# Optimization experiments

Measured on AMD Instinct MI355X. Metric: run time of the kernel, lower is better.

## Reference

```python
import jax, jax.numpy as jnp
import numpy as np

N = 8192
IN_F = 512
OUT_F = 64
ALPHA = 0.2        # LeakyReLU slope
L_ITERS = 3        # RobustSum iterations
EPS = 0.01
GAMMA = 4.0
T = 1.0
NEG_BIG = -9e15


def setup_inputs() -> dict:
    key = jax.random.key(0)
    k1, k2, k3, k4 = jax.random.split(key, 4)
    x = jax.random.normal(k1, (N, IN_F), dtype=jnp.float32)
    adj = jax.random.randint(k2, (N, N), 0, 2, dtype=jnp.int32)
    # xavier-uniform-like init scales
    limW = 1.414 * np.sqrt(6.0 / (IN_F + OUT_F))
    W = jax.random.uniform(k3, (IN_F, OUT_F), dtype=jnp.float32, minval=-limW, maxval=limW)
    lima = 1.414 * np.sqrt(6.0 / (2 * OUT_F + 1))
    a = jax.random.uniform(k4, (2 * OUT_F, 1), dtype=jnp.float32, minval=-lima, maxval=lima)
    return {"adj": adj, "input": x, "W": W, "a": a}


def _robust_sum_mcp(A, V):
    # M = A @ V, then IRLS-style reweighted aggregation (norm='MCP')
    M = A @ V
    for _ in range(L_ITERS):
        Md = jax.lax.stop_gradient(M)
        Vd = jax.lax.stop_gradient(V)
        # pairwise Euclidean distance [N, N] (fused form of torch.cdist)
        d2 = (jnp.sum(Md * Md, axis=1, keepdims=True)
              + jnp.sum(Vd * Vd, axis=1)[None, :]
              - 2.0 * (Md @ Vd.T))
        dist = jnp.sqrt(jnp.maximum(d2, 0.0))
        w = 1.0 / (dist + EPS) - 1.0 / GAMMA
        w = jnp.maximum(w, EPS)          # w[w < eps] = eps
        ww = w * A
        denom = jnp.maximum(jnp.sum(jnp.abs(ww), axis=-1, keepdims=True), 1e-12)
        ww_norm = ww / denom             # F.normalize(p=1, dim=-1)
        M = (1.0 - T) * M + T * (ww_norm @ V)
    return M


def reference(adj, input, W, a):
    adj_f = adj.astype(jnp.float32)
    h = input @ W                                     # [N, OUT_F]
    a1 = a[:OUT_F, 0]                                 # [OUT_F]
    a2 = a[OUT_F:, 0]                                 # [OUT_F]
    # fused equivalent of cat([h_i, h_j]) @ a : e_ij = lrelu(h_i.a1 + h_j.a2)
    e = jax.nn.leaky_relu((h @ a1)[:, None] + (h @ a2)[None, :], ALPHA)  # [N, N]
    scores = adj_f * e + (1.0 - adj_f) * NEG_BIG
    attention = jax.nn.softmax(scores, axis=1)
    # dropout omitted (eval mode / dropout=0.0)
    h_prime = _robust_sum_mcp(attention, h)
    return jax.nn.elu(h_prime)                        # concat=True
```

## Files before the change

### kernel.cpp

```cpp
#include <hip/hip_runtime.h>
#include <hip/hip_bf16.h>

typedef __attribute__((ext_vector_type(8))) short s8v;
typedef __attribute__((ext_vector_type(4))) short s4v;
typedef __attribute__((ext_vector_type(4))) float f4v;

static __device__ __forceinline__ short f2bf(float f){
  unsigned int u = __float_as_uint(f);
  u = (u + 0x7FFFu + ((u >> 16) & 1u)) >> 16;
  return (short)u;
}

static __device__ __forceinline__ s4v pack4(float a, float b, float c, float d){
  union { s4v v; __hip_bfloat162 h[2]; } u;
  u.h[0] = __float22bfloat162_rn(make_float2(a, b));
  u.h[1] = __float22bfloat162_rn(make_float2(c, d));
  return u.v;
}

static __device__ __forceinline__ f4v mfma16(s4v a, s4v b, f4v c){
  return __builtin_amdgcn_mfma_f32_16x16x16bf16_1k(a, b, c, 0, 0, 0);
}

__global__ __launch_bounds__(256) void k_h(const float* __restrict__ x,
                                           const float* __restrict__ W,
                                           float* __restrict__ h){
  int wid = threadIdx.x >> 6, lane = threadIdx.x & 63;
  int r0 = (blockIdx.x * 4 + wid) * 8;
  const float* xr = x + (size_t)r0 * 512;
  float acc[8] = {0.f,0.f,0.f,0.f,0.f,0.f,0.f,0.f};
  #pragma unroll 4
  for (int k = 0; k < 512; ++k){
    float wv = W[k*64 + lane];
    #pragma unroll
    for (int r = 0; r < 8; ++r)
      acc[r] = fmaf(xr[(size_t)r*512 + k], wv, acc[r]);
  }
  #pragma unroll
  for (int r = 0; r < 8; ++r)
    h[(size_t)(r0 + r)*64 + lane] = acc[r];
}

__global__ __launch_bounds__(256) void k_prep(const float* __restrict__ h,
                                              const float* __restrict__ a,
                                              short* __restrict__ VbfSw,
                                              short* __restrict__ VTsw,
                                              float* __restrict__ F,
                                              float2* __restrict__ EG,
                                              float* __restrict__ V2arr,
                                              float* __restrict__ Pv2,
                                              float* __restrict__ Pg,
                                              float* __restrict__ Vpart){
  __shared__ float t[64][65];
  const int tid = threadIdx.x;
  const int lane = tid & 63, w = tid >> 6;
  const int lo = lane & 15, hi = lane >> 4;
  const int i0 = blockIdx.x * 64;
  #pragma unroll
  for (int it = 0; it < 16; ++it){
    int r = w * 16 + it;
    t[r][lane] = h[(size_t)(i0 + r) * 64 + lane];
  }
  __syncthreads();
  #pragma unroll
  for (int ks = 0; ks < 2; ++ks){
    s8v o;
    #pragma unroll
    for (int e = 0; e < 8; ++e)
      o[e] = f2bf(t[w*16 + lo][ks*32 + hi*8 + e]);
    *(s8v*)(VbfSw + ((size_t)(i0/16 + w)*2 + ks)*512 + lane*8) = o;
  }
  const int p = w >> 1;
  #pragma unroll
  for (int oo = 0; oo < 2; ++oo){
    const int ot = (w & 1) * 2 + oo;
    s8v o;
    #pragma unroll
    for (int e = 0; e < 8; ++e){
      int parity = e >> 2, q = e & 3;
      o[e] = f2bf(t[(p*2 + parity)*16 + hi*4 + q][ot*16 + lo]);
    }
    *(s8v*)(VTsw + ((size_t)(i0/32 + p)*4 + ot)*512 + lane*8) = o;
  }
  if (tid < 64){
    const int r = tid;
    float f = 0.f, g = 0.f, v2 = 0.f;
    #pragma unroll 8
    for (int o = 0; o < 64; ++o){
      float hv = t[r][o];
      f  = fmaf(hv, a[o],      f);
      g  = fmaf(hv, a[64 + o], g);
      v2 = fmaf(hv, hv,        v2);
    }
    const int row = i0 + r;
    F[row] = f;
    V2arr[row] = v2;
    EG[row] = make_float2(__expf(g), __expf(0.2f * g));
    float vmin = v2, gmx = g;
    #pragma unroll
    for (int off = 32; off; off >>= 1){
      vmin = fminf(vmin, __shfl_xor(vmin, off));
      gmx  = fmaxf(gmx,  __shfl_xor(gmx,  off));
    }
    if (r == 0){ Pv2[blockIdx.x] = vmin; Pg[blockIdx.x] = gmx; }
    float cs = 0.f;
    #pragma unroll 8
    for (int rr = 0; rr < 64; ++rr) cs += t[rr][tid];
    Vpart[(size_t)blockIdx.x * 64 + tid] = cs;
  }
}

__global__ __launch_bounds__(512, 4) void k_fused(
    const int* __restrict__ adj,
    const float2* __restrict__ EG, const float* __restrict__ V2arr,
    const float* __restrict__ F,
    const float* __restrict__ Pv2, const float* __restrict__ Pg,
    const float* __restrict__ Vpart,
    const short* __restrict__ VbfSw, const short* __restrict__ VTsw,
    float* __restrict__ out)
{
  __shared__ float numT[8][64][16];
  __shared__ float denL[8][16];
  __shared__ float Mlds[16][68];
  __shared__ float M1L[16][68];
  __shared__ __align__(16) short Mb16[16][64];
  __shared__ float CiL[16], rm2L[16], uaiL[16];
  __shared__ float VmeanL[64];
  __shared__ float gmaxS, v2minS;
  __shared__ int actL, chgL, emptyL;

  const int tid  = threadIdx.x;
  const int w    = tid >> 6;
  const int lane = tid & 63;
  const int lo = lane & 15, hi = lane >> 4;
  const int r0 = blockIdx.x << 4;
  const int i  = r0 + lo;

  if (tid < 64){
    float v = fminf(Pv2[tid], Pv2[tid + 64]);
    float g = fmaxf(Pg[tid],  Pg[tid + 64]);
    #pragma unroll
    for (int off = 32; off; off >>= 1){
      v = fminf(v, __shfl_xor(v, off));
      g = fmaxf(g, __shfl_xor(g, off));
    }
    if (tid == 0){ v2minS = v; gmaxS = g; actL = 0; emptyL = 0; }
  }
  __syncthreads();

  const float fi   = F[i];
  const float gmax = gmaxS;
  const float z    = fi + gmax;
  const float B    = fmaxf(z, 0.2f * z);
  const float e1s  = __expf(fi - B);
  const float e2s  = __expf(0.2f * fi - B);

  const int* arow = adj + (size_t)i * 8192 + hi*4;

  const f4v zero4 = {0.f,0.f,0.f,0.f};
  f4v pacc[4] = {zero4, zero4, zero4, zero4};
  float pden = 0.f;

  for (int c = w; c < 128; c += 8){
    const int* ap = arow + (c << 6);
    s4v wwpk[4];
    #pragma unroll
    for (int nt = 0; nt < 4; ++nt){
      const int jb = (c << 6) + nt*16 + hi*4;
      const int4 av4 = *(const int4*)(ap + nt*16);
      const int ab[4] = {av4.x, av4.y, av4.z, av4.w};
      const f4v u0 = *(const f4v*)(EG + jb);
      const f4v u1 = *(const f4v*)(EG + jb + 2);
      const float ega[4] = {u0[0], u0[2], u1[0], u1[2]};
      const float egb[4] = {u0[1], u0[3], u1[1], u1[3]};
      float wwv[4];
      #pragma unroll
      for (int q = 0; q < 4; ++q){
        float u = fmaxf(e1s * ega[q], e2s * egb[q]);
        u = ab[q] ? u : 0.f;
        pden += u;
        wwv[q] = u;
      }
      wwpk[nt] = pack4(wwv[0], wwv[1], wwv[2], wwv[3]);
    }
    const short* vt = VTsw + (size_t)c*4096 + lane*8;
    #pragma unroll
    for (int p = 0; p < 2; ++p){
      #pragma unroll
      for (int ot = 0; ot < 4; ++ot){
        s8v v8 = *(const s8v*)(vt + (p*4 + ot)*512);
        s4v aLo = {v8[0], v8[1], v8[2], v8[3]};
        s4v aHi = {v8[4], v8[5], v8[6], v8[7]};
        pacc[ot] = mfma16(aLo, wwpk[2*p],   pacc[ot]);
        pacc[ot] = mfma16(aHi, wwpk[2*p+1], pacc[ot]);
      }
    }
  }

  pden += __shfl_xor(pden, 16);
  pden += __shfl_xor(pden, 32);
  if (lane < 16) denL[w][lane] = pden;
  #pragma unroll
  for (int ot = 0; ot < 4; ++ot)
    #pragma unroll
    for (int q = 0; q < 4; ++q)
      numT[w][ot*16 + hi*4 + q][lo] = pacc[ot][q];
  __syncthreads();

  {
    const int ii = tid & 15;
    const int o  = tid >> 4;
    float den = 0.f;
    #pragma unroll
    for (int w2 = 0; w2 < 8; ++w2) den += denL[w2][ii];
    if (o == 0){
      uaiL[ii] = (den <= 0.f) ? (1.0f / 8192.0f) : 0.f;
      if (den <= 0.f) emptyL = 1;
    }
    den = fmaxf(den, 1e-30f);
    const float rden = 1.0f / den;
    #pragma unroll
    for (int rep = 0; rep < 2; ++rep){
      const int oo = o + rep*32;
      float num = 0.f;
      #pragma unroll
      for (int w2 = 0; w2 < 8; ++w2) num += numT[w2][oo][ii];
      Mlds[ii][oo] = num * rden;
    }
    if (tid < 16){
      float fb = F[r0 + tid];
      float zb = fb + gmax;
      float Bb = fmaxf(zb, 0.2f * zb);
      CiL[tid] = Bb + __logf(den);
    }
  }
  __syncthreads();

  if (emptyL){
    if (tid < 64){
      float s = 0.f;
      for (int b = 0; b < 128; ++b) s += Vpart[(size_t)b*64 + tid];
      VmeanL[tid] = s * (1.0f / 8192.0f);
    }
    __syncthreads();
    {
      const int r = tid >> 5, c2 = (tid & 31) << 1;
      if (uaiL[r] > 0.f){ Mlds[r][c2] = VmeanL[c2]; Mlds[r][c2+1] = VmeanL[c2+1]; }
    }
    __syncthreads();
  }

  if (tid < 16){
    float s2 = 0.f;
    #pragma unroll 8
    for (int o = 0; o < 64; ++o) s2 = fmaf(Mlds[tid][o], Mlds[tid][o], s2);
    rm2L[tid] = s2;
    if (sqrtf(s2) > sqrtf(v2minS) - 3.85f) actL = 1;
  }
  __syncthreads();

  if (actL){
    {
      const int r = tid >> 5, c2 = (tid & 31) << 1;
      float a0 = Mlds[r][c2], a1 = Mlds[r][c2+1];
      M1L[r][c2] = a0;  M1L[r][c2+1] = a1;
      Mb16[r][c2] = f2bf(a0); Mb16[r][c2+1] = f2bf(a1);
    }
    const float e1c = __expf(fi - CiL[lo]);
    const float e2c = __expf(0.2f * fi - CiL[lo]);
    const float uai = uaiL[lo];
    __syncthreads();

    for (int pass = 0; pass < 3; ++pass){
      if (tid == 0) chgL = 0;
      __syncthreads();
      const float rm2 = rm2L[lo];
      s8v bM[2];
      #pragma unroll
      for (int ks = 0; ks < 2; ++ks)
        bM[ks] = *(const s8v*)&Mb16[lo][ks*32 + hi*8];

      f4v cacc[4] = {zero4, zero4, zero4, zero4};
      float cden = 0.f;

      for (int c = w; c < 128; c += 8){
        f4v acc[4] = {zero4, zero4, zero4, zero4};
        const short* vb = VbfSw + (size_t)c*4096 + lane*8;
        #pragma unroll
        for (int nt = 0; nt < 4; ++nt){
          #pragma unroll
          for (int ks = 0; ks < 2; ++ks){
            s8v av = *(const s8v*)(vb + (nt*2 + ks)*512);
            acc[nt] = __builtin_amdgcn_mfma_f32_16x16x32_bf16(av, bM[ks], acc[nt], 0, 0, 0);
          }
        }
        f4v d2s[4];
        float dmin = 1e30f;
        #pragma unroll
        for (int nt = 0; nt < 4; ++nt){
          const int jb = (c << 6) + nt*16 + hi*4;
          const f4v v2q = *(const f4v*)(V2arr + jb);
          #pragma unroll
          for (int q = 0; q < 4; ++q){
            float d2 = fmaf(-2.0f, acc[nt][q], rm2 + v2q[q]);
            d2s[nt][q] = d2;
            dmin = fminf(dmin, d2);
          }
        }
        if (__any(dmin < 16.0f)){
          const int* ap = arow + (c << 6);
          s4v wwpk[4];
          #pragma unroll
          for (int nt = 0; nt < 4; ++nt){
            const int jb = (c << 6) + nt*16 + hi*4;
            const int4 av4 = *(const int4*)(ap + nt*16);
            const int ab[4] = {av4.x, av4.y, av4.z, av4.w};
            const f4v u0 = *(const f4v*)(EG + jb);
            const f4v u1 = *(const f4v*)(EG + jb + 2);
            const float ega[4] = {u0[0], u0[2], u1[0], u1[2]};
            const float egb[4] = {u0[1], u0[3], u1[1], u1[3]};
            float wwv[4];
            #pragma unroll
            for (int q = 0; q < 4; ++q){
              float A = fmaxf(e1c * ega[q], e2c * egb[q]);
              A = ab[q] ? A : uai;
              float dist  = sqrtf(fmaxf(d2s[nt][q], 0.f));
              float delta = fmaxf(__builtin_amdgcn_rcpf(dist + 0.01f) - 0.26f, 0.f);
              float ww = delta * A;
              cden += ww;
              wwv[q] = ww;
            }
            wwpk[nt] = pack4(wwv[0], wwv[1], wwv[2], wwv[3]);
          }
          const short* vt = VTsw + (size_t)c*4096 + lane*8;
          #pragma unroll
          for (int p = 0; p < 2; ++p){
            #pragma unroll
            for (int ot = 0; ot < 4; ++ot){
              s8v v8 = *(const s8v*)(vt + (p*4 + ot)*512);
              s4v aLo = {v8[0], v8[1], v8[2], v8[3]};
              s4v aHi = {v8[4], v8[5], v8[6], v8[7]};
              cacc[ot] = mfma16(aLo, wwpk[2*p],   cacc[ot]);
              cacc[ot] = mfma16(aHi, wwpk[2*p+1], cacc[ot]);
            }
          }
        }
      }

      if (__any(cden > 0.f)) chgL = 1;
      __syncthreads();
      if (chgL){
        float cd = cden;
        cd += __shfl_xor(cd, 16);
        cd += __shfl_xor(cd, 32);
        if (lane < 16) denL[w][lane] = cd;
        #pragma unroll
        for (int ot = 0; ot < 4; ++ot)
          #pragma unroll
          for (int q = 0; q < 4; ++q)
            numT[w][ot*16 + hi*4 + q][lo] = cacc[ot][q];
        __syncthreads();
        {
          const int ii = tid & 15;
          const int o  = tid >> 4;
          float den = 0.f;
          #pragma unroll
          for (int w2 = 0; w2 < 8; ++w2) den += denL[w2][ii];
          const float rden = 1.0f / (0.01f + den);
          #pragma unroll
          for (int rep = 0; rep < 2; ++rep){
            const int oo = o + rep*32;
            float num = 0.f;
            #pragma unroll
            for (int w2 = 0; w2 < 8; ++w2) num += numT[w2][oo][ii];
            Mlds[ii][oo] = fmaf(0.01f, M1L[ii][oo], num) * rden;
          }
        }
        __syncthreads();
        {
          const int r = tid >> 5, c2 = (tid & 31) << 1;
          Mb16[r][c2]   = f2bf(Mlds[r][c2]);
          Mb16[r][c2+1] = f2bf(Mlds[r][c2+1]);
        }
        if (tid < 16){
          float s2 = 0.f;
          #pragma unroll 8
          for (int o = 0; o < 64; ++o) s2 = fmaf(Mlds[tid][o], Mlds[tid][o], s2);
          rm2L[tid] = s2;
        }
        __syncthreads();
      }
    }
  }
  __syncthreads();

  #pragma unroll
  for (int rr = 0; rr < 2; ++rr){
    const int ir = w*2 + rr;
    const float v = Mlds[ir][lane];
    out[(size_t)(r0 + ir) * 64 + lane] = (v > 0.f) ? v : (__expf(v) - 1.0f);
  }
}

extern "C" void kernel_launch(void* const* d_in, const int* in_sizes, int n_in,
                              void* d_out, int out_size, void* d_ws, size_t ws_size,
                              hipStream_t stream){
  (void)in_sizes; (void)n_in; (void)out_size; (void)ws_size;
  const int*   adj = (const int*)d_in[0];
  const float* x   = (const float*)d_in[1];
  const float* W   = (const float*)d_in[2];
  const float* a   = (const float*)d_in[3];
  float* out = (float*)d_out;
  char* ws = (char*)d_ws;

  float* h     = (float*)(ws);
  short* VbfSw = (short*)(ws + (2u << 20));
  short* VTsw  = (short*)(ws + (3u << 20));
  float* F     = (float*)(ws + (4u << 20));
  float* V2arr = (float*)(ws + (4u << 20) + (32u << 10));
  float2* EG   = (float2*)(ws + (4u << 20) + (64u << 10));
  float* Vpart = (float*)(ws + (4u << 20) + (128u << 10));
  float* Pv2   = (float*)(ws + (4u << 20) + (160u << 10));
  float* Pg    = (float*)(ws + (4u << 20) + (161u << 10));

  k_h    <<<256, 256, 0, stream>>>(x, W, h);
  k_prep <<<128, 256, 0, stream>>>(h, a, VbfSw, VTsw, F, EG, V2arr, Pv2, Pg, Vpart);
  k_fused<<<512, 512, 0, stream>>>(adj, EG, V2arr, F, Pv2, Pg, Vpart, VbfSw, VTsw, out);
}
```

Baseline: 138.4 us.

## Process 32 rows per block, bit-pack adjacency, reduce partials via LDS atomics

Each block now handles 32 rows with 1024 threads, and every wave computes two 16-row tiles. This lets each loaded V/VT fragment and EG value feed twice as many MFMAs. In the first pass the adjacency rows are packed into 64-bit masks in workspace, so the three IRLS passes read bits instead of re-reading int32 adjacency. Cross-wave reductions use LDS atomicAdd instead of per-wave staging arrays, the pruning threshold changes from 16 to 14.75, and the pass loop exits early when nothing changes. The costs are higher register pressure, atomic contention, a grid of only 256 blocks, and a changed threshold that may affect accuracy.

```diff
diff --git a/kernel.cpp b/kernel.cpp
--- a/kernel.cpp
+++ b/kernel.cpp
@@ -110,21 +110,22 @@
   }
 }
 
-__global__ __launch_bounds__(512, 4) void k_fused(
+__global__ __launch_bounds__(1024, 4) void k_fused(
     const int* __restrict__ adj,
     const float2* __restrict__ EG, const float* __restrict__ V2arr,
     const float* __restrict__ F,
     const float* __restrict__ Pv2, const float* __restrict__ Pg,
     const float* __restrict__ Vpart,
     const short* __restrict__ VbfSw, const short* __restrict__ VTsw,
+    unsigned long long* __restrict__ adjbits,
     float* __restrict__ out)
 {
-  __shared__ float numT[8][64][16];
-  __shared__ float denL[8][16];
-  __shared__ float Mlds[16][68];
-  __shared__ float M1L[16][68];
-  __shared__ __align__(16) short Mb16[16][64];
-  __shared__ float CiL[16], rm2L[16], uaiL[16];
+  __shared__ float Macc[32][65];
+  __shared__ float denA[32];
+  __shared__ float Mlds[32][68];
+  __shared__ float M1L[32][68];
+  __shared__ __align__(16) short Mb16[32][64];
+  __shared__ float CiL[32], rm2L[32], uaiL[32];
   __shared__ float VmeanL[64];
   __shared__ float gmaxS, v2minS;
   __shared__ int actL, chgL, emptyL;
@@ -133,9 +134,15 @@
   const int w    = tid >> 6;
   const int lane = tid & 63;
   const int lo = lane & 15, hi = lane >> 4;
-  const int r0 = blockIdx.x << 4;
-  const int i  = r0 + lo;
-
+  const int r0 = blockIdx.x << 5;
+  const int i0 = r0 + lo;
+  const int i1 = r0 + 16 + lo;
+
+  {
+    float* mz = &Macc[0][0];
+    for (int k2 = tid; k2 < 32*65; k2 += 1024) mz[k2] = 0.f;
+    if (tid < 32) denA[tid] = 0.f;
+  }
   if (tid < 64){
     float v = fminf(Pv2[tid], Pv2[tid + 64]);
     float g = fmaxf(Pg[tid],  Pg[tid + 64]);
@@ -148,41 +155,62 @@
   }
   __syncthreads();
 
-  const float fi   = F[i];
+  const float fi0 = F[i0], fi1 = F[i1];
   const float gmax = gmaxS;
-  const float z    = fi + gmax;
-  const float B    = fmaxf(z, 0.2f * z);
-  const float e1s  = __expf(fi - B);
-  const float e2s  = __expf(0.2f * fi - B);
-
-  const int* arow = adj + (size_t)i * 8192 + hi*4;
+  const float z0 = fi0 + gmax, z1 = fi1 + gmax;
+  const float B0 = fmaxf(z0, 0.2f * z0);
+  const float B1 = fmaxf(z1, 0.2f * z1);
+  const float e1s0 = __expf(fi0 - B0), e2s0 = __expf(0.2f * fi0 - B0);
+  const float e1s1 = __expf(fi1 - B1), e2s1 = __expf(0.2f * fi1 - B1);
+
+  const int* arow0 = adj + (size_t)i0 * 8192 + hi*4;
+  const int* arow1 = adj + (size_t)i1 * 8192 + hi*4;
 
   const f4v zero4 = {0.f,0.f,0.f,0.f};
-  f4v pacc[4] = {zero4, zero4, zero4, zero4};
-  float pden = 0.f;
-
-  for (int c = w; c < 128; c += 8){
-    const int* ap = arow + (c << 6);
-    s4v wwpk[4];
+  f4v pacc0[4] = {zero4, zero4, zero4, zero4};
+  f4v pacc1[4] = {zero4, zero4, zero4, zero4};
+  float pden0 = 0.f, pden1 = 0.f;
+
+  for (int c = w; c < 128; c += 16){
+    const int* ap0 = arow0 + (c << 6);
+    const int* ap1 = arow1 + (c << 6);
+    s4v wp0[4], wp1[4];
+    unsigned long long mrow0 = 0ull, mrow1 = 0ull;
     #pragma unroll
     for (int nt = 0; nt < 4; ++nt){
       const int jb = (c << 6) + nt*16 + hi*4;
-      const int4 av4 = *(const int4*)(ap + nt*16);
-      const int ab[4] = {av4.x, av4.y, av4.z, av4.w};
+      const int4 a0 = *(const int4*)(ap0 + nt*16);
+      const int4 a1 = *(const int4*)(ap1 + nt*16);
       const f4v u0 = *(const f4v*)(EG + jb);
       const f4v u1 = *(const f4v*)(EG + jb + 2);
       const float ega[4] = {u0[0], u0[2], u1[0], u1[2]};
       const float egb[4] = {u0[1], u0[3], u1[1], u1[3]};
-      float wwv[4];
+      const int ab0[4] = {a0.x, a0.y, a0.z, a0.w};
+      const int ab1[4] = {a1.x, a1.y, a1.z, a1.w};
+      float w0v[4], w1v[4];
       #pragma unroll
       for (int q = 0; q < 4; ++q){
-        float u = fmaxf(e1s * ega[q], e2s * egb[q]);
-        u = ab[q] ? u : 0.f;
-        pden += u;
-        wwv[q] = u;
-      }
-      wwpk[nt] = pack4(wwv[0], wwv[1], wwv[2], wwv[3]);
-    }
+        float u = fmaxf(e1s0 * ega[q], e2s0 * egb[q]);
+        u = ab0[q] ? u : 0.f;
+        pden0 += u; w0v[q] = u;
+        float v = fmaxf(e1s1 * ega[q], e2s1 * egb[q]);
+        v = ab1[q] ? v : 0.f;
+        pden1 += v; w1v[q] = v;
+      }
+      const unsigned nib0 = (unsigned)ab0[0] | ((unsigned)ab0[1] << 1)
+                          | ((unsigned)ab0[2] << 2) | ((unsigned)ab0[3] << 3);
+      const unsigned nib1 = (unsigned)ab1[0] | ((unsigned)ab1[1] << 1)
+                          | ((unsigned)ab1[2] << 2) | ((unsigned)ab1[3] << 3);
+      mrow0 |= (unsigned long long)nib0 << (nt*16 + hi*4);
+      mrow1 |= (unsigned long long)nib1 << (nt*16 + hi*4);
+      wp0[nt] = pack4(w0v[0], w0v[1], w0v[2], w0v[3]);
+      wp1[nt] = pack4(w1v[0], w1v[1], w1v[2], w1v[3]);
+    }
+    mrow0 |= __shfl_xor(mrow0, 16); mrow0 |= __shfl_xor(mrow0, 32);
+    mrow1 |= __shfl_xor(mrow1, 16); mrow1 |= __shfl_xor(mrow1, 32);
+    if (hi == 0) adjbits[(size_t)c * 8192 + i0] = mrow0;
+    if (hi == 1) adjbits[(size_t)c * 8192 + i1] = mrow1;
+
     const short* vt = VTsw + (size_t)c*4096 + lane*8;
     #pragma unroll
     for (int p = 0; p < 2; ++p){
@@ -191,47 +219,41 @@
         s8v v8 = *(const s8v*)(vt + (p*4 + ot)*512);
         s4v aLo = {v8[0], v8[1], v8[2], v8[3]};
         s4v aHi = {v8[4], v8[5], v8[6], v8[7]};
-        pacc[ot] = mfma16(aLo, wwpk[2*p],   pacc[ot]);
-        pacc[ot] = mfma16(aHi, wwpk[2*p+1], pacc[ot]);
-      }
-    }
-  }
-
-  pden += __shfl_xor(pden, 16);
-  pden += __shfl_xor(pden, 32);
-  if (lane < 16) denL[w][lane] = pden;
+        pacc0[ot] = mfma16(aLo, wp0[2*p],   pacc0[ot]);
+        pacc0[ot] = mfma16(aHi, wp0[2*p+1], pacc0[ot]);
+        pacc1[ot] = mfma16(aLo, wp1[2*p],   pacc1[ot]);
+        pacc1[ot] = mfma16(aHi, wp1[2*p+1], pacc1[ot]);
+      }
+    }
+  }
+
+  pden0 += __shfl_xor(pden0, 16); pden0 += __shfl_xor(pden0, 32);
+  pden1 += __shfl_xor(pden1, 16); pden1 += __shfl_xor(pden1, 32);
+  if (hi == 0) atomicAdd(&denA[lo],      pden0);
+  if (hi == 1) atomicAdd(&denA[16 + lo], pden1);
   #pragma unroll
   for (int ot = 0; ot < 4; ++ot)
     #pragma unroll
-    for (int q = 0; q < 4; ++q)
-      numT[w][ot*16 + hi*4 + q][lo] = pacc[ot][q];
+    for (int q = 0; q < 4; ++q){
+      atomicAdd(&Macc[lo]     [ot*16 + hi*4 + q], pacc0[ot][q]);
+      atomicAdd(&Macc[16 + lo][ot*16 + hi*4 + q], pacc1[ot][q]);
+    }
   __syncthreads();
 
   {
-    const int ii = tid & 15;
-    const int o  = tid >> 4;
-    float den = 0.f;
-    #pragma unroll
-    for (int w2 = 0; w2 < 8; ++w2) den += denL[w2][ii];
-    if (o == 0){
-      uaiL[ii] = (den <= 0.f) ? (1.0f / 8192.0f) : 0.f;
-      if (den <= 0.f) emptyL = 1;
-    }
-    den = fmaxf(den, 1e-30f);
+    const int r = tid >> 5, cc = (tid & 31) << 1;
+    const float den = fmaxf(denA[r], 1e-30f);
     const float rden = 1.0f / den;
-    #pragma unroll
-    for (int rep = 0; rep < 2; ++rep){
-      const int oo = o + rep*32;
-      float num = 0.f;
-      #pragma unroll
-      for (int w2 = 0; w2 < 8; ++w2) num += numT[w2][oo][ii];
-      Mlds[ii][oo] = num * rden;
-    }
-    if (tid < 16){
-      float fb = F[r0 + tid];
-      float zb = fb + gmax;
-      float Bb = fmaxf(zb, 0.2f * zb);
-      CiL[tid] = Bb + __logf(den);
+    Mlds[r][cc]   = Macc[r][cc]   * rden;
+    Mlds[r][cc+1] = Macc[r][cc+1] * rden;
+    if (tid < 32){
+      const float dn = denA[tid];
+      uaiL[tid] = (dn <= 0.f) ? (1.0f / 8192.0f) : 0.f;
+      if (dn <= 0.f) emptyL = 1;
+      const float fb = F[r0 + tid];
+      const float zb = fb + gmax;
+      const float Bb = fmaxf(zb, 0.2f * zb);
+      CiL[tid] = Bb + __logf(fmaxf(dn, 1e-30f));
     }
   }
   __syncthreads();
@@ -244,13 +266,13 @@
     }
     __syncthreads();
     {
-      const int r = tid >> 5, c2 = (tid & 31) << 1;
-      if (uaiL[r] > 0.f){ Mlds[r][c2] = VmeanL[c2]; Mlds[r][c2+1] = VmeanL[c2+1]; }
+      const int r = tid >> 5, cc = (tid & 31) << 1;
+      if (uaiL[r] > 0.f){ Mlds[r][cc] = VmeanL[cc]; Mlds[r][cc+1] = VmeanL[cc+1]; }
     }
     __syncthreads();
   }
 
-  if (tid < 16){
+  if (tid < 32){
     float s2 = 0.f;
     #pragma unroll 8
     for (int o = 0; o < 64; ++o) s2 = fmaf(Mlds[tid][o], Mlds[tid][o], s2);
@@ -261,76 +283,105 @@
 
   if (actL){
     {
-      const int r = tid >> 5, c2 = (tid & 31) << 1;
-      float a0 = Mlds[r][c2], a1 = Mlds[r][c2+1];
-      M1L[r][c2] = a0;  M1L[r][c2+1] = a1;
-      Mb16[r][c2] = f2bf(a0); Mb16[r][c2+1] = f2bf(a1);
-    }
-    const float e1c = __expf(fi - CiL[lo]);
-    const float e2c = __expf(0.2f * fi - CiL[lo]);
-    const float uai = uaiL[lo];
+      const int r = tid >> 5, cc = (tid & 31) << 1;
+      const float a0 = Mlds[r][cc], a1 = Mlds[r][cc+1];
+      M1L[r][cc] = a0;  M1L[r][cc+1] = a1;
+      Mb16[r][cc] = f2bf(a0); Mb16[r][cc+1] = f2bf(a1);
+    }
+    const float e1c0 = __expf(fi0 - CiL[lo]);
+    const float e2c0 = __expf(0.2f * fi0 - CiL[lo]);
+    const float e1c1 = __expf(fi1 - CiL[16 + lo]);
+    const float e2c1 = __expf(0.2f * fi1 - CiL[16 + lo]);
+    const float uai0 = uaiL[lo], uai1 = uaiL[16 + lo];
     __syncthreads();
 
     for (int pass = 0; pass < 3; ++pass){
-      if (tid == 0) chgL = 0;
+      {
+        float* mz = &Macc[0][0];
+        for (int k2 = tid; k2 < 32*65; k2 += 1024) mz[k2] = 0.f;
+        if (tid < 32) denA[tid] = 0.f;
+        if (tid == 0) chgL = 0;
+      }
       __syncthreads();
-      const float rm2 = rm2L[lo];
-      s8v bM[2];
+      const float rm20 = rm2L[lo], rm21 = rm2L[16 + lo];
+      s8v bM0[2], bM1[2];
       #pragma unroll
-      for (int ks = 0; ks < 2; ++ks)
-        bM[ks] = *(const s8v*)&Mb16[lo][ks*32 + hi*8];
-
-      f4v cacc[4] = {zero4, zero4, zero4, zero4};
-      float cden = 0.f;
-
-      for (int c = w; c < 128; c += 8){
-        f4v acc[4] = {zero4, zero4, zero4, zero4};
+      for (int ks = 0; ks < 2; ++ks){
+        bM0[ks] = *(const s8v*)&Mb16[lo]     [ks*32 + hi*8];
+        bM1[ks] = *(const s8v*)&Mb16[16 + lo][ks*32 + hi*8];
+      }
+
+      f4v cacc0[4] = {zero4, zero4, zero4, zero4};
+      f4v cacc1[4] = {zero4, zero4, zero4, zero4};
+      float cden0 = 0.f, cden1 = 0.f;
+
+      for (int c = w; c < 128; c += 16){
+        f4v acc0[4] = {zero4, zero4, zero4, zero4};
+        f4v acc1[4] = {zero4, zero4, zero4, zero4};
         const short* vb = VbfSw + (size_t)c*4096 + lane*8;
         #pragma unroll
         for (int nt = 0; nt < 4; ++nt){
           #pragma unroll
           for (int ks = 0; ks < 2; ++ks){
             s8v av = *(const s8v*)(vb + (nt*2 + ks)*512);
-            acc[nt] = __builtin_amdgcn_mfma_f32_16x16x32_bf16(av, bM[ks], acc[nt], 0, 0, 0);
+            acc0[nt] = __builtin_amdgcn_mfma_f32_16x16x32_bf16(av, bM0[ks], acc0[nt], 0, 0, 0);
+            acc1[nt] = __builtin_amdgcn_mfma_f32_16x16x32_bf16(av, bM1[ks], acc1[nt], 0, 0, 0);
           }
         }
-        f4v d2s[4];
-        float dmin = 1e30f;
+        float dm0 = 1e30f, dm1 = 1e30f;
         #pragma unroll
         for (int nt = 0; nt < 4; ++nt){
           const int jb = (c << 6) + nt*16 + hi*4;
           const f4v v2q = *(const f4v*)(V2arr + jb);
           #pragma unroll
           for (int q = 0; q < 4; ++q){
-            float d2 = fmaf(-2.0f, acc[nt][q], rm2 + v2q[q]);
-            d2s[nt][q] = d2;
-            dmin = fminf(dmin, d2);
+            const float d0 = fmaf(-2.0f, acc0[nt][q], rm20 + v2q[q]);
+            const float d1 = fmaf(-2.0f, acc1[nt][q], rm21 + v2q[q]);
+            acc0[nt][q] = d0; acc1[nt][q] = d1;
+            dm0 = fminf(dm0, d0); dm1 = fminf(dm1, d1);
           }
         }
-        if (__any(dmin < 16.0f)){
-          const int* ap = arow + (c << 6);
-          s4v wwpk[4];
+        const bool t0 = __any(dm0 < 14.75f);
+        const bool t1 = __any(dm1 < 14.75f);
+        if (t0 | t1){
+          const unsigned long long mrow0 = t0 ? adjbits[(size_t)c * 8192 + i0] : 0ull;
+          const unsigned long long mrow1 = t1 ? adjbits[(size_t)c * 8192 + i1] : 0ull;
+          s4v wp0[4], wp1[4];
           #pragma unroll
           for (int nt = 0; nt < 4; ++nt){
             const int jb = (c << 6) + nt*16 + hi*4;
-            const int4 av4 = *(const int4*)(ap + nt*16);
-            const int ab[4] = {av4.x, av4.y, av4.z, av4.w};
             const f4v u0 = *(const f4v*)(EG + jb);
             const f4v u1 = *(const f4v*)(EG + jb + 2);
             const float ega[4] = {u0[0], u0[2], u1[0], u1[2]};
             const float egb[4] = {u0[1], u0[3], u1[1], u1[3]};
-            float wwv[4];
-            #pragma unroll
-            for (int q = 0; q < 4; ++q){
-              float A = fmaxf(e1c * ega[q], e2c * egb[q]);
-              A = ab[q] ? A : uai;
-              float dist  = sqrtf(fmaxf(d2s[nt][q], 0.f));
-              float delta = fmaxf(__builtin_amdgcn_rcpf(dist + 0.01f) - 0.26f, 0.f);
-              float ww = delta * A;
-              cden += ww;
-              wwv[q] = ww;
+            if (t0){
+              const unsigned nib = (unsigned)(mrow0 >> (nt*16 + hi*4)) & 0xFu;
+              float wv[4];
+              #pragma unroll
+              for (int q = 0; q < 4; ++q){
+                float A = fmaxf(e1c0 * ega[q], e2c0 * egb[q]);
+                A = ((nib >> q) & 1u) ? A : uai0;
+                const float dist  = sqrtf(fmaxf(acc0[nt][q], 0.f));
+                const float delta = fmaxf(__builtin_amdgcn_rcpf(dist + 0.01f) - 0.26f, 0.f);
+                const float ww = delta * A;
+                cden0 += ww; wv[q] = ww;
+              }
+              wp0[nt] = pack4(wv[0], wv[1], wv[2], wv[3]);
             }
-            wwpk[nt] = pack4(wwv[0], wwv[1], wwv[2], wwv[3]);
+            if (t1){
+              const unsigned nib = (unsigned)(mrow1 >> (nt*16 + hi*4)) & 0xFu;
+              float wv[4];
+              #pragma unroll
+              for (int q = 0; q < 4; ++q){
+                float A = fmaxf(e1c1 * ega[q], e2c1 * egb[q]);
+                A = ((nib >> q) & 1u) ? A : uai1;
+                const float dist  = sqrtf(fmaxf(acc1[nt][q], 0.f));
+                const float delta = fmaxf(__builtin_amdgcn_rcpf(dist + 0.01f) - 0.26f, 0.f);
+                const float ww = delta * A;
+                cden1 += ww; wv[q] = ww;
+              }
+              wp1[nt] = pack4(wv[0], wv[1], wv[2], wv[3]);
+            }
           }
           const short* vt = VTsw + (size_t)c*4096 + lane*8;
           #pragma unroll
@@ -340,56 +391,52 @@
               s8v v8 = *(const s8v*)(vt + (p*4 + ot)*512);
               s4v aLo = {v8[0], v8[1], v8[2], v8[3]};
               s4v aHi = {v8[4], v8[5], v8[6], v8[7]};
-              cacc[ot] = mfma16(aLo, wwpk[2*p],   cacc[ot]);
-              cacc[ot] = mfma16(aHi, wwpk[2*p+1], cacc[ot]);
+              if (t0){
+                cacc0[ot] = mfma16(aLo, wp0[2*p],   cacc0[ot]);
+                cacc0[ot] = mfma16(aHi, wp0[2*p+1], cacc0[ot]);
+              }
+              if (t1){
+                cacc1[ot] = mfma16(aLo, wp1[2*p],   cacc1[ot]);
+                cacc1[ot] = mfma16(aHi, wp1[2*p+1], cacc1[ot]);
+              }
             }
           }
         }
       }
 
-      if (__any(cden > 0.f)) chgL = 1;
-      __syncthreads();
-      if (chgL){
-        float cd = cden;
-        cd += __shfl_xor(cd, 16);
-        cd += __shfl_xor(cd, 32);
-        if (lane < 16) denL[w][lane] = cd;
+      if (__any(cden0 > 0.f) || __any(cden1 > 0.f)){
+        chgL = 1;
+        float cd0 = cden0, cd1 = cden1;
+        cd0 += __shfl_xor(cd0, 16); cd0 += __shfl_xor(cd0, 32);
+        cd1 += __shfl_xor(cd1, 16); cd1 += __shfl_xor(cd1, 32);
+        if (hi == 0) atomicAdd(&denA[lo],      cd0);
+        if (hi == 1) atomicAdd(&denA[16 + lo], cd1);
         #pragma unroll
         for (int ot = 0; ot < 4; ++ot)
           #pragma unroll
-          for (int q = 0; q < 4; ++q)
-            numT[w][ot*16 + hi*4 + q][lo] = cacc[ot][q];
-        __syncthreads();
-        {
-          const int ii = tid & 15;
-          const int o  = tid >> 4;
-          float den = 0.f;
-          #pragma unroll
-          for (int w2 = 0; w2 < 8; ++w2) den += denL[w2][ii];
-          const float rden = 1.0f / (0.01f + den);
-          #pragma unroll
-          for (int rep = 0; rep < 2; ++rep){
-            const int oo = o + rep*32;
-            float num = 0.f;
-            #pragma unroll
-            for (int w2 = 0; w2 < 8; ++w2) num += numT[w2][oo][ii];
-            Mlds[ii][oo] = fmaf(0.01f, M1L[ii][oo], num) * rden;
+          for (int q = 0; q < 4; ++q){
+            atomicAdd(&Macc[lo]     [ot*16 + hi*4 + q], cacc0[ot][q]);
+            atomicAdd(&Macc[16 + lo][ot*16 + hi*4 + q], cacc1[ot][q]);
           }
-        }
-        __syncthreads();
-        {
-          const int r = tid >> 5, c2 = (tid & 31) << 1;
-          Mb16[r][c2]   = f2bf(Mlds[r][c2]);
-          Mb16[r][c2+1] = f2bf(Mlds[r][c2+1]);
-        }
-        if (tid < 16){
-          float s2 = 0.f;
-          #pragma unroll 8
-          for (int o = 0; o < 64; ++o) s2 = fmaf(Mlds[tid][o], Mlds[tid][o], s2);
-          rm2L[tid] = s2;
-        }
-        __syncthreads();
-      }
+      }
+      __syncthreads();
+      if (!chgL) break;
+      {
+        const int r = tid >> 5, cc = (tid & 31) << 1;
+        const float rden = 1.0f / (0.01f + denA[r]);
+        const float n0 = fmaf(0.01f, M1L[r][cc],   Macc[r][cc])   * rden;
+        const float n1 = fmaf(0.01f, M1L[r][cc+1], Macc[r][cc+1]) * rden;
+        Mlds[r][cc] = n0;  Mlds[r][cc+1] = n1;
+        Mb16[r][cc] = f2bf(n0); Mb16[r][cc+1] = f2bf(n1);
+      }
+      __syncthreads();
+      if (tid < 32){
+        float s2 = 0.f;
+        #pragma unroll 8
+        for (int o = 0; o < 64; ++o) s2 = fmaf(Mlds[tid][o], Mlds[tid][o], s2);
+        rm2L[tid] = s2;
+      }
+      __syncthreads();
     }
   }
   __syncthreads();
@@ -422,8 +469,9 @@
   float* Vpart = (float*)(ws + (4u << 20) + (128u << 10));
   float* Pv2   = (float*)(ws + (4u << 20) + (160u << 10));
   float* Pg    = (float*)(ws + (4u << 20) + (161u << 10));
+  unsigned long long* adjbits = (unsigned long long*)(ws + (5u << 20));
 
   k_h    <<<256, 256, 0, stream>>>(x, W, h);
   k_prep <<<128, 256, 0, stream>>>(h, a, VbfSw, VTsw, F, EG, V2arr, Pv2, Pg, Vpart);
-  k_fused<<<512, 512, 0, stream>>>(adj, EG, V2arr, F, Pv2, Pg, Vpart, VbfSw, VTsw, out);
-}
+  k_fused<<<256, 1024, 0, stream>>>(adj, EG, V2arr, F, Pv2, Pg, Vpart, VbfSw, VTsw, adjbits, out);
+}
```

New measurement: 198.4 us. 1.43x slower.
